# Performance work log

Hardware: AMD Instinct MI355X
Metric: run time of the kernel (lower is better)

The kernel has to match this reference:

```python
import jax, jax.numpy as jnp
import numpy as np

IN_SIZE = 1024
HIDDEN = 50
OUT_DIM = 8
BATCH = 16384
BN_EPS = 1e-5


def _gf(h, W1, b1, W2, b2):
    # graph_fusion: Linear -> LeakyReLU(0.2) -> Linear -> Tanh
    t = h @ W1 + b1
    t = jnp.where(t > 0, t, 0.2 * t)
    return jnp.tanh(t @ W2 + b2)


def _lrelu(z):
    return jnp.where(z > 0, z, 0.01 * z)  # F.leaky_relu default slope


def _dot(p, q):
    return jnp.sum(p * q, axis=-1)  # batched [B,1,D]@[B,D,1] -> [B]


def setup_inputs() -> dict:
    key = jax.random.key(0)
    ks = jax.random.split(key, 16)
    d, h, o = IN_SIZE, HIDDEN, OUT_DIM
    s = lambda n: 1.0 / np.sqrt(n)
    return {
        "x": jax.random.normal(ks[0], (BATCH, 3, d), jnp.float32),
        "att_W": jax.random.normal(ks[1], (d, 1), jnp.float32) * s(d),
        "att_b": jnp.zeros((1,), jnp.float32),
        "gf_W1": jax.random.normal(ks[2], (2 * d, 64), jnp.float32) * s(2 * d),
        "gf_b1": jnp.zeros((64,), jnp.float32),
        "gf_W2": jax.random.normal(ks[3], (64, d), jnp.float32) * s(64),
        "gf_b2": jnp.zeros((d,), jnp.float32),
        "bn_gamma": jnp.ones((3 * d,), jnp.float32),
        "bn_beta": jnp.zeros((3 * d,), jnp.float32),
        "l1_W": jax.random.normal(ks[4], (3 * d, h), jnp.float32) * s(3 * d),
        "l1_b": jnp.zeros((h,), jnp.float32),
        "l2_W": jax.random.normal(ks[5], (h, h), jnp.float32) * s(h),
        "l2_b": jnp.zeros((h,), jnp.float32),
        "l3_W": jax.random.normal(ks[6], (h, o), jnp.float32) * s(h),
        "l3_b": jnp.zeros((o,), jnp.float32),
    }


def _forward(x, att_W, att_b, gf_W1, gf_b1, gf_W2, gf_b2,
             bn_gamma, bn_beta, l1_W, l1_b, l2_W, l2_b, l3_W, l3_b):
    a1, v1, l1_ = x[:, 0, :], x[:, 1, :], x[:, 2, :]
    gf = lambda p, q: _gf(jnp.concatenate([p, q], axis=1), gf_W1, gf_b1, gf_W2, gf_b2)

    # unimodal attention weights, softmax over the 3 modalities
    att = jnp.tanh(x @ att_W + att_b)[..., 0]          # [B,3]
    w_uni = jax.nn.softmax(att, axis=1)                # [B,3]
    sa, sv, sl = w_uni[:, 0], w_uni[:, 1], w_uni[:, 2]
    unimodal = (sa[:, None] * a1 + sv[:, None] * v1 + sl[:, None] * l1_) / 3.0

    a = jax.nn.softmax(a1, axis=1)
    v = jax.nn.softmax(v1, axis=1)
    l = jax.nn.softmax(l1_, axis=1)
    sav = (sa + sv) / (_dot(a, v) + 0.5)
    sal = (sa + sl) / (_dot(a, l) + 0.5)
    svl = (sl + sv) / (_dot(v, l) + 0.5)
    w_bi = jax.nn.softmax(jnp.stack([sav, sal, svl], axis=1), axis=1)  # [B,3]

    a_v = _lrelu(w_bi[:, 0:1] * gf(a1, v1))
    a_l = _lrelu(w_bi[:, 1:2] * gf(a1, l1_))
    v_l = _lrelu(w_bi[:, 2:3] * gf(v1, l1_))
    bimodal = (a_v + a_l + v_l) / 3.0

    a_v2 = jax.nn.softmax(a_v, axis=1)
    a_l2 = jax.nn.softmax(a_l, axis=1)
    v_l2 = jax.nn.softmax(v_l, axis=1)
    savvl = (sav + svl) / (_dot(a_v2, v_l2) + 0.5)
    saavl = (sav + sal) / (_dot(a_v2, a_l2) + 0.5)
    savll = (sal + svl) / (_dot(a_l2, v_l2) + 0.5)
    savl = (sav + sl) / (_dot(a_v2, l) + 0.5)
    salv = (sal + sv) / (_dot(a_l2, v) + 0.5)
    svla = (sa + svl) / (_dot(v_l2, a) + 0.5)
    w_tri = jax.nn.softmax(
        jnp.stack([savvl, saavl, savll, savl, salv, svla], axis=1), axis=1)  # [B,6]

    avvl = _lrelu(w_tri[:, 0:1] * gf(a_v, v_l))
    aavl = _lrelu(w_tri[:, 1:2] * gf(a_v, a_l))
    avll = _lrelu(w_tri[:, 2:3] * gf(v_l, a_l))
    avl = _lrelu(w_tri[:, 3:4] * gf(a_v, l1_))
    alv = _lrelu(w_tri[:, 4:5] * gf(a_l, v1))
    vla = _lrelu(w_tri[:, 5:6] * gf(v_l, a1))
    trimodal = (avvl + aavl + avll + avl + alv + vla) / 6.0

    fusion = jnp.concatenate([unimodal, bimodal, trimodal], axis=1)  # [B,3*in]
    # BatchNorm1d in eval mode: running_mean=0, running_var=1
    fusion = fusion * (bn_gamma / jnp.sqrt(1.0 + BN_EPS)) + bn_beta
    y = jnp.tanh(fusion @ l1_W + l1_b)
    y = jnp.tanh(y @ l2_W + l2_b)
    y2 = jax.nn.softmax(y @ l3_W + l3_b, axis=1)
    total_weights = jnp.concatenate([w_uni, w_bi, w_tri], axis=1)  # [B,12]
    return y2, total_weights


def reference(x, att_W, att_b, gf_W1, gf_b1, gf_W2, gf_b2,
              bn_gamma, bn_beta, l1_W, l1_b, l2_W, l2_b, l3_W, l3_b):
    return _forward(x, att_W, att_b, gf_W1, gf_b1, gf_W2, gf_b2,
                    bn_gamma, bn_beta, l1_W, l1_b, l2_W, l2_b, l3_W, l3_b)
```

## Files before the change

kernel.cpp:

```cpp
#include <hip/hip_runtime.h>
#include <math.h>

#define NB 16384
#define DD 1024
#define KF 5120

typedef unsigned short u16;
typedef unsigned int u32;
typedef __attribute__((ext_vector_type(8))) short bf16x8;
typedef __attribute__((ext_vector_type(4))) float f32x4;

__device__ __forceinline__ float bf2f(u16 u){
  return __uint_as_float(((unsigned)u) << 16);
}
__device__ __forceinline__ u16 f2bf(float f){
  unsigned u = __float_as_uint(f);
  return (u16)((u + 0x7fffu + ((u >> 16) & 1u)) >> 16);
}
__device__ __forceinline__ u16 f2bf_tr(float f){
  return (u16)(__float_as_uint(f) >> 16);
}
__device__ __forceinline__ float fast_tanh(float x){
  float e = __expf(2.0f * x);
  return 1.0f - 2.0f * __builtin_amdgcn_rcpf(e + 1.0f);
}
__device__ __forceinline__ float wredsum(float x){
  #pragma unroll
  for(int o = 32; o >= 1; o >>= 1) x += __shfl_xor(x, o);
  return x;
}
__device__ __forceinline__ float wredmax(float x){
  #pragma unroll
  for(int o = 32; o >= 1; o >>= 1) x = fmaxf(x, __shfl_xor(x, o));
  return x;
}
__device__ __forceinline__ bf16x8 pack8f(float4 f0, float4 f1){
  bf16x8 r;
  r[0]=(short)f2bf(f0.x); r[1]=(short)f2bf(f0.y); r[2]=(short)f2bf(f0.z); r[3]=(short)f2bf(f0.w);
  r[4]=(short)f2bf(f1.x); r[5]=(short)f2bf(f1.y); r[6]=(short)f2bf(f1.z); r[7]=(short)f2bf(f1.w);
  return r;
}
__device__ __forceinline__ void gll16(const void* g, void* l){
  __builtin_amdgcn_global_load_lds(
      (const __attribute__((address_space(1))) u32*)g,
      (__attribute__((address_space(3))) u32*)l, 16, 0, 0);
}

__global__ __launch_bounds__(256) void k1_stats(
    const float* __restrict__ x, const float* __restrict__ attW,
    const float* __restrict__ attb, float* __restrict__ stats,
    u16* __restrict__ Fcat, float* __restrict__ tw)
{
  int wave = threadIdx.x >> 6, lane = threadIdx.x & 63;
  int r = blockIdx.x * 4 + wave;
  const float* xr = x + (size_t)r * 3 * DD;
  float a[16], v[16], l[16];
  float dA=0.f,dV=0.f,dL=0.f, mA=-1e30f,mV=-1e30f,mL=-1e30f;
  #pragma unroll
  for(int i = 0; i < 16; i++){
    int k = lane + i*64;
    a[i] = xr[k]; v[i] = xr[DD+k]; l[i] = xr[2*DD+k];
    float w = attW[k];
    dA = fmaf(a[i], w, dA); dV = fmaf(v[i], w, dV); dL = fmaf(l[i], w, dL);
    mA = fmaxf(mA, a[i]); mV = fmaxf(mV, v[i]); mL = fmaxf(mL, l[i]);
  }
  dA = wredsum(dA); dV = wredsum(dV); dL = wredsum(dL);
  mA = wredmax(mA); mV = wredmax(mV); mL = wredmax(mL);

  float Sa=0.f,Sv=0.f,Sl=0.f,Eav=0.f,Eal=0.f,Evl=0.f;
  #pragma unroll
  for(int i = 0; i < 16; i++){
    float ea = __expf(a[i]-mA), ev = __expf(v[i]-mV), el = __expf(l[i]-mL);
    Sa += ea; Sv += ev; Sl += el;
    Eav += ea*ev; Eal += ea*el; Evl += ev*el;
  }
  Sa = wredsum(Sa); Sv = wredsum(Sv); Sl = wredsum(Sl);
  Eav = wredsum(Eav); Eal = wredsum(Eal); Evl = wredsum(Evl);

  float ab = attb[0];
  float ta = fast_tanh(dA + ab), tv = fast_tanh(dV + ab), tl = fast_tanh(dL + ab);
  float mm = fmaxf(ta, fmaxf(tv, tl));
  float e0 = __expf(ta-mm), e1 = __expf(tv-mm), e2 = __expf(tl-mm);
  float ss = e0 + e1 + e2;
  float sa = e0/ss, sv = e1/ss, sl = e2/ss;
  float dav = Eav/(Sa*Sv), dal = Eal/(Sa*Sl), dvl = Evl/(Sv*Sl);
  float sav = (sa+sv)/(dav+0.5f);
  float sal = (sa+sl)/(dal+0.5f);
  float svl = (sv+sl)/(dvl+0.5f);
  float m2 = fmaxf(sav, fmaxf(sal, svl));
  float f0 = __expf(sav-m2), f1 = __expf(sal-m2), f2 = __expf(svl-m2);
  float s2 = f0 + f1 + f2;
  float wb0 = f0/s2, wb1 = f1/s2, wb2 = f2/s2;

  if(lane == 0){
    float* st = stats + (size_t)r*24;
    st[0]=sa; st[1]=sv; st[2]=sl;
    st[3]=wb0; st[4]=wb1; st[5]=wb2;
    st[6]=sav; st[7]=sal; st[8]=svl;
    st[9]=mA; st[10]=Sa; st[11]=mV; st[12]=Sv; st[13]=mL; st[14]=Sl;
    float* twr = tw + (size_t)r*12;
    twr[0]=sa; twr[1]=sv; twr[2]=sl; twr[3]=wb0; twr[4]=wb1; twr[5]=wb2;
  }
  #pragma unroll
  for(int i = 0; i < 16; i++){
    int k = lane + i*64;
    Fcat[(size_t)r*KF + k] = f2bf((sa*a[i] + sv*v[i] + sl*l[i]) * (1.0f/3.0f));
  }
}

__global__ __launch_bounds__(256) void kprew_b1(
    const float* __restrict__ W1, u16* __restrict__ Wb1)
{
  int idx = blockIdx.x * 256 + threadIdx.x;
  int n = idx >> 10, k = idx & 1023;
  float v = (n < 64) ? W1[(size_t)k*64 + n] : W1[(size_t)(1024+k)*64 + (n-64)];
  Wb1[idx] = f2bf(v);
}

__global__ __launch_bounds__(256) void kprew_w2t(
    const float* __restrict__ W2, u16* __restrict__ W2T)
{
  int idx = blockIdx.x * 256 + threadIdx.x;
  int c = idx >> 6, k = idx & 63;
  W2T[idx] = f2bf(W2[(size_t)k*DD + c]);
}

template<int FROM_X>
__global__ __launch_bounds__(256) void kg1v2(
    const float* __restrict__ xf, const u16* __restrict__ fc,
    const u16* __restrict__ Wb1, float* __restrict__ UV)
{
  __shared__ u16 Asm[2][64*64];
  int tid = threadIdx.x;
  int wv = tid >> 6, lane = tid & 63;
  int fr = lane & 15, kg = lane >> 4;
  int mb = blockIdx.x * 64;

  const u16* gsrc0 = nullptr; const u16* gsrc1 = nullptr;
  const float* xsrc0 = nullptr; const float* xsrc1 = nullptr;
  int rr_ = tid >> 3, pp_ = tid & 7;
  int sp_ = pp_ ^ (rr_ & 7);
  if(FROM_X){
    xsrc0 = xf + (size_t)(mb + rr_)*1024 + pp_*8;
    xsrc1 = xf + (size_t)(mb + rr_ + 32)*1024 + pp_*8;
  } else {
    int r8 = lane >> 3, p = lane & 7;
    int sp = p ^ (r8 & 7);
    int m0 = mb + (2*wv)*8 + r8;
    int m1 = mb + (2*wv+1)*8 + r8;
    int R0 = m0/3, R1 = m1/3;
    gsrc0 = fc + (size_t)R0*KF + (size_t)(1 + (m0 - 3*R0))*1024 + sp*8;
    gsrc1 = fc + (size_t)R1*KF + (size_t)(1 + (m1 - 3*R1))*1024 + sp*8;
  }

  f32x4 acc[4][2];
  #pragma unroll
  for(int rf = 0; rf < 4; rf++)
    #pragma unroll
    for(int nf = 0; nf < 2; nf++) acc[rf][nf] = (f32x4){0.f,0.f,0.f,0.f};

  if(FROM_X){
    float4 a0 = *(const float4*)xsrc0, a1 = *(const float4*)(xsrc0+4);
    float4 c0 = *(const float4*)xsrc1, c1 = *(const float4*)(xsrc1+4);
    *(bf16x8*)&Asm[0][rr_*64 + sp_*8]      = pack8f(a0,a1);
    *(bf16x8*)&Asm[0][(rr_+32)*64 + sp_*8] = pack8f(c0,c1);
  } else {
    gll16(gsrc0, &Asm[0][(2*wv)*512]);
    gll16(gsrc1, &Asm[0][(2*wv+1)*512]);
  }
  __syncthreads();

  int buf = 0;
  for(int ci = 0; ci < 16; ci++){
    int k0 = ci*64;
    float4 na0, na1, nc0, nc1;
    if(ci < 15){
      if(FROM_X){
        na0 = *(const float4*)(xsrc0 + k0 + 64); na1 = *(const float4*)(xsrc0 + k0 + 68);
        nc0 = *(const float4*)(xsrc1 + k0 + 64); nc1 = *(const float4*)(xsrc1 + k0 + 68);
      } else {
        gll16(gsrc0 + k0 + 64, &Asm[buf^1][(2*wv)*512]);
        gll16(gsrc1 + k0 + 64, &Asm[buf^1][(2*wv+1)*512]);
      }
    }
    #pragma unroll
    for(int ks = 0; ks < 2; ks++){
      bf16x8 a[4];
      #pragma unroll
      for(int rf = 0; rf < 4; rf++){
        int row = rf*16 + fr;
        int slot = (ks*4 + kg) ^ (fr & 7);
        a[rf] = *(const bf16x8*)&Asm[buf][row*64 + slot*8];
      }
      #pragma unroll
      for(int nf = 0; nf < 2; nf++){
        int col = wv*32 + nf*16 + fr;
        bf16x8 b = *(const bf16x8*)&Wb1[(size_t)col*1024 + k0 + ks*32 + kg*8];
        #pragma unroll
        for(int rf = 0; rf < 4; rf++)
          acc[rf][nf] = __builtin_amdgcn_mfma_f32_16x16x32_bf16(a[rf], b, acc[rf][nf], 0, 0, 0);
      }
    }
    if(FROM_X && ci < 15){
      *(bf16x8*)&Asm[buf^1][rr_*64 + sp_*8]      = pack8f(na0,na1);
      *(bf16x8*)&Asm[buf^1][(rr_+32)*64 + sp_*8] = pack8f(nc0,nc1);
    }
    __syncthreads();
    buf ^= 1;
  }

  #pragma unroll
  for(int rf = 0; rf < 4; rf++)
    #pragma unroll
    for(int nf = 0; nf < 2; nf++)
      #pragma unroll
      for(int q = 0; q < 4; q++)
        UV[(size_t)(mb + rf*16 + kg*4 + q)*128 + wv*32 + nf*16 + fr] = acc[rf][nf][q];
}

template<int P, int SUM>
__global__ __launch_bounds__(256) void kL2v2(
    const float* __restrict__ UVA, const float* __restrict__ UVB,
    const u16* __restrict__ W2T, const float* __restrict__ b1,
    const float* __restrict__ b2, const float* __restrict__ stats,
    u16* __restrict__ Fcat)
{
  __shared__ u16 Tsm[P][16][64];
  __shared__ float stw[16][8];
  int tid = threadIdx.x;
  int wv = tid >> 6, lane = tid & 63;
  int fr = lane & 15, kg = lane >> 4;
  int Rb = blockIdx.x * 16;
  int cb = blockIdx.y * 256 + wv * 64;

  const int NG = P*16*8;
  for(int i = tid; i < NG; i += 256){
    int g = i & 7, r = (i >> 3) & 15, p = i >> 7;
    int R = Rb + r;
    int up, vp; const float* VBb;
    if(P == 3){
      up = (p == 2) ? 1 : 0;
      vp = (p == 0) ? 1 : 2;
      VBb = UVA;
    } else {
      up = (0x210200 >> (p*4)) & 15;
      vp = (0x012112 >> (p*4)) & 15;
      VBb = (p < 3) ? UVA : UVB;
    }
    const float* Up = UVA + (size_t)(3*R + up)*128 + g*8;
    const float* Vp = VBb + (size_t)(3*R + vp)*128 + 64 + g*8;
    float4 u0 = *(const float4*)Up, u1 = *(const float4*)(Up+4);
    float4 v0 = *(const float4*)Vp, v1 = *(const float4*)(Vp+4);
    float4 bb0 = *(const float4*)(b1 + g*8), bb1 = *(const float4*)(b1 + g*8 + 4);
    float t[8] = {u0.x+v0.x+bb0.x, u0.y+v0.y+bb0.y, u0.z+v0.z+bb0.z, u0.w+v0.w+bb0.w,
                  u1.x+v1.x+bb1.x, u1.y+v1.y+bb1.y, u1.z+v1.z+bb1.z, u1.w+v1.w+bb1.w};
    bf16x8 o;
    #pragma unroll
    for(int j = 0; j < 8; j++){
      float tv = t[j] > 0.f ? t[j] : 0.2f*t[j];
      o[j] = (short)f2bf_tr(tv);
    }
    *(bf16x8*)&Tsm[p][r][(g ^ (r & 7))*8] = o;
  }
  if(tid < 16*P){
    int r = tid / P, p = tid - r*P;
    stw[r][p] = stats[(size_t)(Rb + r)*24 + (SUM ? 15 : 3) + p];
  }
  __syncthreads();

  f32x4 acc[P][4];
  #pragma unroll
  for(int p = 0; p < P; p++)
    #pragma unroll
    for(int cf = 0; cf < 4; cf++) acc[p][cf] = (f32x4){0.f,0.f,0.f,0.f};

  #pragma unroll
  for(int ks = 0; ks < 2; ks++){
    bf16x8 a[P];
    #pragma unroll
    for(int p = 0; p < P; p++)
      a[p] = *(const bf16x8*)&Tsm[p][fr][(((ks<<2)+kg) ^ (fr & 7))*8];
    #pragma unroll
    for(int cf = 0; cf < 4; cf++){
      bf16x8 b = *(const bf16x8*)&W2T[(size_t)(cb + cf*16 + fr)*64 + ks*32 + kg*8];
      #pragma unroll
      for(int p = 0; p < P; p++)
        acc[p][cf] = __builtin_amdgcn_mfma_f32_16x16x32_bf16(a[p], b, acc[p][cf], 0, 0, 0);
    }
  }

  #pragma unroll
  for(int q = 0; q < 4; q++){
    int Rq = Rb + kg*4 + q;
    #pragma unroll
    for(int cf = 0; cf < 4; cf++){
      int c = cb + cf*16 + fr;
      float b2c = b2[c];
      if(SUM){
        float s = 0.f;
        #pragma unroll
        for(int p = 0; p < P; p++){
          float g = stw[kg*4+q][p] * fast_tanh(acc[p][cf][q] + b2c);
          s += g > 0.f ? g : 0.01f*g;
        }
        Fcat[(size_t)Rq*KF + 4096 + c] = f2bf(s * (1.0f/6.0f));
      } else {
        #pragma unroll
        for(int p = 0; p < P; p++){
          float g = stw[kg*4+q][p] * fast_tanh(acc[p][cf][q] + b2c);
          float val = g > 0.f ? g : 0.01f*g;
          Fcat[(size_t)Rq*KF + (size_t)(1+p)*1024 + c] = f2bf(val);
        }
      }
    }
  }
}

__global__ __launch_bounds__(256) void k3s_stats2(
    const u16* __restrict__ Fcat, const float* __restrict__ x,
    float* __restrict__ stats, float* __restrict__ tw)
{
  int wave = threadIdx.x >> 6, lane = threadIdx.x & 63;
  int r = blockIdx.x * 4 + wave;
  const u16*   pv = Fcat + (size_t)r*KF + 1024;
  const float* xr = x    + (size_t)3*r*DD;
  float av[16], al[16], vl[16];
  float mav=-1e30f, mal=-1e30f, mvl=-1e30f;
  #pragma unroll
  for(int i = 0; i < 16; i++){
    int k = lane + i*64;
    av[i] = bf2f(pv[k]); al[i] = bf2f(pv[DD+k]); vl[i] = bf2f(pv[2*DD+k]);
    mav = fmaxf(mav, av[i]); mal = fmaxf(mal, al[i]); mvl = fmaxf(mvl, vl[i]);
  }
  mav = wredmax(mav); mal = wredmax(mal); mvl = wredmax(mvl);

  float* st = stats + (size_t)r*24;
  float sa=st[0], sv=st[1], sl=st[2];
  float sav=st[6], sal=st[7], svl=st[8];
  float mA=st[9], Sa=st[10], mV=st[11], Sv=st[12], mL=st[13], Sl=st[14];

  float Savv=0.f,Sall=0.f,Svll=0.f,E1=0.f,E2=0.f,E3=0.f,E4=0.f,E5=0.f,E6=0.f;
  #pragma unroll
  for(int i = 0; i < 16; i++){
    int k = lane + i*64;
    float a1 = xr[k], v1 = xr[DD+k], l1 = xr[2*DD+k];
    float eav = __expf(av[i]-mav), eal = __expf(al[i]-mal), evl = __expf(vl[i]-mvl);
    Savv += eav; Sall += eal; Svll += evl;
    float ea = __expf(a1-mA), ev = __expf(v1-mV), el = __expf(l1-mL);
    E1 += eav*evl; E2 += eav*eal; E3 += eal*evl;
    E4 += eav*el;  E5 += eal*ev;  E6 += evl*ea;
  }
  Savv = wredsum(Savv); Sall = wredsum(Sall); Svll = wredsum(Svll);
  E1 = wredsum(E1); E2 = wredsum(E2); E3 = wredsum(E3);
  E4 = wredsum(E4); E5 = wredsum(E5); E6 = wredsum(E6);

  float d1 = E1/(Savv*Svll), d2 = E2/(Savv*Sall), d3 = E3/(Sall*Svll);
  float d4 = E4/(Savv*Sl),   d5 = E5/(Sall*Sv),   d6 = E6/(Svll*Sa);
  float t0 = (sav+svl)/(d1+0.5f);
  float t1 = (sav+sal)/(d2+0.5f);
  float t2 = (sal+svl)/(d3+0.5f);
  float t3 = (sav+sl)/(d4+0.5f);
  float t4 = (sal+sv)/(d5+0.5f);
  float t5 = (sa+svl)/(d6+0.5f);
  float mx = fmaxf(fmaxf(fmaxf(t0,t1),fmaxf(t2,t3)),fmaxf(t4,t5));
  float g0=__expf(t0-mx),g1=__expf(t1-mx),g2=__expf(t2-mx);
  float g3=__expf(t3-mx),g4=__expf(t4-mx),g5=__expf(t5-mx);
  float gs = g0+g1+g2+g3+g4+g5;
  if(lane == 0){
    float wt[6] = {g0/gs,g1/gs,g2/gs,g3/gs,g4/gs,g5/gs};
    float* twr = tw + (size_t)r*12;
    #pragma unroll
    for(int p = 0; p < 6; p++){ st[15+p] = wt[p]; twr[6+p] = wt[p]; }
  }
}

__global__ __launch_bounds__(256) void k6_prew(
    const float* __restrict__ gamma, const float* __restrict__ l1W,
    u16* __restrict__ WpT)
{
  int kk = blockIdx.x * 256 + threadIdx.x;
  int j  = blockIdx.y;
  const float gsc = 1.0f / sqrtf(1.0f + 1e-5f);
  int korig; float sc;
  if(kk < 1024){ korig = kk; sc = 1.f; }
  else if(kk < 4096){ korig = 1024 + ((kk - 1024) & 1023); sc = 1.0f/3.0f; }
  else { korig = 2048 + (kk - 4096); sc = 1.f; }
  float v = (j < 50) ? l1W[(size_t)korig*50 + j] * gamma[korig] * gsc * sc : 0.f;
  WpT[(size_t)j*KF + kk] = f2bf(v);
}

__global__ __launch_bounds__(256) void k6_preb(
    const float* __restrict__ beta, const float* __restrict__ l1W,
    const float* __restrict__ l1b, float* __restrict__ bp)
{
  __shared__ float red[4][64];
  int j = threadIdx.x & 63, seg = threadIdx.x >> 6;
  float s = 0.f;
  if(j < 50){
    for(int k = seg*768; k < seg*768 + 768; k++)
      s = fmaf(beta[k], l1W[(size_t)k*50 + j], s);
  }
  red[seg][j] = s;
  __syncthreads();
  if(seg == 0){
    float t = red[0][j] + red[1][j] + red[2][j] + red[3][j];
    bp[j] = (j < 50) ? (l1b[j] + t) : 0.f;
  }
}

__global__ __launch_bounds__(256) void k6v3(
    const u16* __restrict__ Fcat, const u16* __restrict__ WpT,
    const float* __restrict__ bp,
    const float* __restrict__ l2W, const float* __restrict__ l2b,
    const float* __restrict__ l3W, const float* __restrict__ l3b,
    float* __restrict__ y2out)
{
  __shared__ __align__(16) char smem[29760];
  u16*  Asm = (u16*)smem;
  float* W2s = (float*)(smem + 8192);
  float* W3s = (float*)(smem + 8192 + 12800);
  float* Ys  = (float*)smem;
  float* Ys2 = (float*)(smem + 8192 + 12800 + 1600);

  int tid = threadIdx.x;
  int wv = tid >> 6, lane = tid & 63;
  int fr = lane & 15, kg = lane >> 4;
  int rb = blockIdx.x * 32;

  for(int t = tid; t < 3200; t += 256){
    int c = t & 63;
    W2s[t] = (c < 50) ? l2W[(t >> 6)*50 + c] : 0.f;
  }
  for(int t = tid; t < 400; t += 256) W3s[t] = l3W[t];

  int r8 = lane >> 3, pp = lane & 7;
  int sp = pp ^ r8;
  const u16* gsrc = Fcat + (size_t)(rb + wv*8 + r8)*KF + sp*8;
  const u16* bptr = WpT  + (size_t)(fr)*KF + (size_t)wv*16*KF + kg*8;

  f32x4 acc[2];
  acc[0] = (f32x4){0.f,0.f,0.f,0.f};
  acc[1] = (f32x4){0.f,0.f,0.f,0.f};

  gll16(gsrc, &Asm[wv*512]);
  __syncthreads();

  int buf = 0;
  for(int ci = 0; ci < 80; ci++){
    int k0 = ci*64;
    if(ci < 79)
      gll16(gsrc + k0 + 64, &Asm[(buf^1)*2048 + wv*512]);
    #pragma unroll
    for(int ks = 0; ks < 2; ks++){
      bf16x8 b = *(const bf16x8*)(bptr + k0 + ks*32);
      #pragma unroll
      for(int rf = 0; rf < 2; rf++){
        int row = rf*16 + fr;
        int slot = (ks*4 + kg) ^ (fr & 7);
        bf16x8 a = *(const bf16x8*)&Asm[buf*2048 + row*64 + slot*8];
        acc[rf] = __builtin_amdgcn_mfma_f32_16x16x32_bf16(a, b, acc[rf], 0, 0, 0);
      }
    }
    __syncthreads();
    buf ^= 1;
  }

  {
    int col = wv*16 + fr;
    float bpc = bp[col];
    #pragma unroll
    for(int rf = 0; rf < 2; rf++)
      #pragma unroll
      for(int q = 0; q < 4; q++){
        int row = rf*16 + kg*4 + q;
        if(col < 50) Ys[row*56 + col] = fast_tanh(acc[rf][q] + bpc);
      }
  }
  __syncthreads();

  {
    int r = tid >> 3, cg = (tid & 7) * 7;
    float a2[7] = {0,0,0,0,0,0,0};
    for(int k = 0; k < 50; k++){
      float yv = Ys[r*56 + k];
      #pragma unroll
      for(int c = 0; c < 7; c++) a2[c] = fmaf(yv, W2s[k*64 + cg + c], a2[c]);
    }
    #pragma unroll
    for(int c = 0; c < 7; c++){
      int cc = cg + c;
      if(cc < 50) Ys2[r*56 + cc] = fast_tanh(a2[c] + l2b[cc]);
    }
  }
  __syncthreads();

  {
    int r = tid >> 3, c = tid & 7;
    float z = l3b[c];
    for(int k = 0; k < 50; k++) z = fmaf(Ys2[r*56 + k], W3s[k*8 + c], z);
    float m = z;
    m = fmaxf(m, __shfl_xor(m, 1));
    m = fmaxf(m, __shfl_xor(m, 2));
    m = fmaxf(m, __shfl_xor(m, 4));
    float e = __expf(z - m);
    float s = e;
    s += __shfl_xor(s, 1); s += __shfl_xor(s, 2); s += __shfl_xor(s, 4);
    y2out[(size_t)(rb + r)*8 + c] = e / s;
  }
}

extern "C" void kernel_launch(void* const* d_in, const int* in_sizes, int n_in,
                              void* d_out, int out_size, void* d_ws, size_t ws_size,
                              hipStream_t stream)
{
  (void)in_sizes; (void)n_in; (void)out_size; (void)ws_size;
  const float* x    = (const float*)d_in[0];
  const float* attW = (const float*)d_in[1];
  const float* attb = (const float*)d_in[2];
  const float* gfW1 = (const float*)d_in[3];
  const float* gfb1 = (const float*)d_in[4];
  const float* gfW2 = (const float*)d_in[5];
  const float* gfb2 = (const float*)d_in[6];
  const float* bng  = (const float*)d_in[7];
  const float* bnb  = (const float*)d_in[8];
  const float* l1W  = (const float*)d_in[9];
  const float* l1b  = (const float*)d_in[10];
  const float* l2W  = (const float*)d_in[11];
  const float* l2b  = (const float*)d_in[12];
  const float* l3W  = (const float*)d_in[13];
  const float* l3b  = (const float*)d_in[14];

  float* out = (float*)d_out;
  float* tw  = out + (size_t)NB*8;

  float* ws    = (float*)d_ws;
  float* stats = ws;
  float* UV1   = stats + (size_t)NB*24;
  float* UV2   = UV1 + (size_t)3*NB*128;
  float* bp    = UV2 + (size_t)3*NB*128;
  u16* WpT     = (u16*)(bp + 64);
  u16* Wb1     = WpT + (size_t)64*KF;
  u16* W2T     = Wb1 + (size_t)128*1024;
  u16* Fcat    = W2T + (size_t)1024*64;

  k1_stats<<<dim3(NB/4), dim3(256), 0, stream>>>(x, attW, attb, stats, Fcat, tw);
  kprew_b1<<<dim3(512), dim3(256), 0, stream>>>(gfW1, Wb1);
  kprew_w2t<<<dim3(256), dim3(256), 0, stream>>>(gfW2, W2T);
  k6_prew<<<dim3(20, 64), dim3(256), 0, stream>>>(bng, l1W, WpT);
  k6_preb<<<dim3(1), dim3(256), 0, stream>>>(bnb, l1W, l1b, bp);

  kg1v2<1><<<dim3(3*NB/64), dim3(256), 0, stream>>>(x, (const u16*)nullptr, Wb1, UV1);
  kL2v2<3,0><<<dim3(NB/16, 4), dim3(256), 0, stream>>>(UV1, UV1, W2T, gfb1, gfb2, stats, Fcat);
  k3s_stats2<<<dim3(NB/4), dim3(256), 0, stream>>>(Fcat, x, stats, tw);
  kg1v2<0><<<dim3(3*NB/64), dim3(256), 0, stream>>>((const float*)nullptr, Fcat, Wb1, UV2);
  kL2v2<6,1><<<dim3(NB/16, 4), dim3(256), 0, stream>>>(UV2, UV1, W2T, gfb1, gfb2, stats, Fcat);
  k6v3<<<dim3(NB/32), dim3(256), 0, stream>>>(Fcat, WpT, bp, l2W, l2b, l3W, l3b, out);
}
```

Before: 424.5 us.

## Stage gf outputs through LDS for coalesced stores and vectorize stats loads

kL2v2 is replaced by kL2v3. Each block now covers all 1024 columns for its 16 rows by looping over four column groups, so the T-tile gather and A-fragment loads happen once per block instead of once per column quarter. Results are staged in a padded LDS buffer and written to Fcat as 16-byte vectors, replacing scattered 2-byte stores. The stats kernels k1_stats and k3s_stats2 switch to float2 and packed-bf16 loads and stores to halve the number of memory instructions. The cost is a quarter as many blocks for the kL2 launches, extra barriers, and more LDS per block, which may lower occupancy.

```diff
diff --git a/kernel.cpp b/kernel.cpp
--- a/kernel.cpp
+++ b/kernel.cpp
@@ -19,6 +19,9 @@
 }
 __device__ __forceinline__ u16 f2bf_tr(float f){
   return (u16)(__float_as_uint(f) >> 16);
+}
+__device__ __forceinline__ u32 pack2bf(float a, float b){
+  return (u32)f2bf(a) | ((u32)f2bf(b) << 16);
 }
 __device__ __forceinline__ float fast_tanh(float x){
   float e = __expf(2.0f * x);
@@ -53,26 +56,33 @@
 {
   int wave = threadIdx.x >> 6, lane = threadIdx.x & 63;
   int r = blockIdx.x * 4 + wave;
-  const float* xr = x + (size_t)r * 3 * DD;
-  float a[16], v[16], l[16];
+  const float2* xr  = (const float2*)(x + (size_t)r * 3 * DD);
+  const float2* aw2 = (const float2*)attW;
+  float2 a[8], v[8], l[8];
   float dA=0.f,dV=0.f,dL=0.f, mA=-1e30f,mV=-1e30f,mL=-1e30f;
   #pragma unroll
-  for(int i = 0; i < 16; i++){
-    int k = lane + i*64;
-    a[i] = xr[k]; v[i] = xr[DD+k]; l[i] = xr[2*DD+k];
-    float w = attW[k];
-    dA = fmaf(a[i], w, dA); dV = fmaf(v[i], w, dV); dL = fmaf(l[i], w, dL);
-    mA = fmaxf(mA, a[i]); mV = fmaxf(mV, v[i]); mL = fmaxf(mL, l[i]);
+  for(int i = 0; i < 8; i++){
+    int k2 = lane + i*64;
+    a[i] = xr[k2]; v[i] = xr[512+k2]; l[i] = xr[1024+k2];
+    float2 w = aw2[k2];
+    dA = fmaf(a[i].x, w.x, fmaf(a[i].y, w.y, dA));
+    dV = fmaf(v[i].x, w.x, fmaf(v[i].y, w.y, dV));
+    dL = fmaf(l[i].x, w.x, fmaf(l[i].y, w.y, dL));
+    mA = fmaxf(mA, fmaxf(a[i].x, a[i].y));
+    mV = fmaxf(mV, fmaxf(v[i].x, v[i].y));
+    mL = fmaxf(mL, fmaxf(l[i].x, l[i].y));
   }
   dA = wredsum(dA); dV = wredsum(dV); dL = wredsum(dL);
   mA = wredmax(mA); mV = wredmax(mV); mL = wredmax(mL);
 
   float Sa=0.f,Sv=0.f,Sl=0.f,Eav=0.f,Eal=0.f,Evl=0.f;
   #pragma unroll
-  for(int i = 0; i < 16; i++){
-    float ea = __expf(a[i]-mA), ev = __expf(v[i]-mV), el = __expf(l[i]-mL);
-    Sa += ea; Sv += ev; Sl += el;
-    Eav += ea*ev; Eal += ea*el; Evl += ev*el;
+  for(int i = 0; i < 8; i++){
+    float eax = __expf(a[i].x-mA), eay = __expf(a[i].y-mA);
+    float evx = __expf(v[i].x-mV), evy = __expf(v[i].y-mV);
+    float elx = __expf(l[i].x-mL), ely = __expf(l[i].y-mL);
+    Sa += eax+eay; Sv += evx+evy; Sl += elx+ely;
+    Eav += eax*evx + eay*evy; Eal += eax*elx + eay*ely; Evl += evx*elx + evy*ely;
   }
   Sa = wredsum(Sa); Sv = wredsum(Sv); Sl = wredsum(Sl);
   Eav = wredsum(Eav); Eal = wredsum(Eal); Evl = wredsum(Evl);
@@ -101,10 +111,13 @@
     float* twr = tw + (size_t)r*12;
     twr[0]=sa; twr[1]=sv; twr[2]=sl; twr[3]=wb0; twr[4]=wb1; twr[5]=wb2;
   }
-  #pragma unroll
-  for(int i = 0; i < 16; i++){
-    int k = lane + i*64;
-    Fcat[(size_t)r*KF + k] = f2bf((sa*a[i] + sv*v[i] + sl*l[i]) * (1.0f/3.0f));
+  u32* uniw = (u32*)(Fcat + (size_t)r*KF);
+  #pragma unroll
+  for(int i = 0; i < 8; i++){
+    int k2 = lane + i*64;
+    float ux = (sa*a[i].x + sv*v[i].x + sl*l[i].x) * (1.0f/3.0f);
+    float uy = (sa*a[i].y + sv*v[i].y + sl*l[i].y) * (1.0f/3.0f);
+    uniw[k2] = pack2bf(ux, uy);
   }
 }
 
@@ -219,19 +232,20 @@
 }
 
 template<int P, int SUM>
-__global__ __launch_bounds__(256) void kL2v2(
+__global__ __launch_bounds__(256) void kL2v3(
     const float* __restrict__ UVA, const float* __restrict__ UVB,
     const u16* __restrict__ W2T, const float* __restrict__ b1,
     const float* __restrict__ b2, const float* __restrict__ stats,
     u16* __restrict__ Fcat)
 {
+  const int NP = SUM ? 1 : P;
   __shared__ u16 Tsm[P][16][64];
+  __shared__ u16 Osm[SUM?1:P][16][264];
   __shared__ float stw[16][8];
   int tid = threadIdx.x;
   int wv = tid >> 6, lane = tid & 63;
   int fr = lane & 15, kg = lane >> 4;
   int Rb = blockIdx.x * 16;
-  int cb = blockIdx.y * 256 + wv * 64;
 
   const int NG = P*16*8;
   for(int i = tid; i < NG; i += 256){
@@ -268,50 +282,67 @@
   }
   __syncthreads();
 
-  f32x4 acc[P][4];
-  #pragma unroll
-  for(int p = 0; p < P; p++)
-    #pragma unroll
-    for(int cf = 0; cf < 4; cf++) acc[p][cf] = (f32x4){0.f,0.f,0.f,0.f};
-
-  #pragma unroll
-  for(int ks = 0; ks < 2; ks++){
-    bf16x8 a[P];
+  bf16x8 afr[2][P];
+  #pragma unroll
+  for(int ks = 0; ks < 2; ks++)
     #pragma unroll
     for(int p = 0; p < P; p++)
-      a[p] = *(const bf16x8*)&Tsm[p][fr][(((ks<<2)+kg) ^ (fr & 7))*8];
-    #pragma unroll
-    for(int cf = 0; cf < 4; cf++){
-      bf16x8 b = *(const bf16x8*)&W2T[(size_t)(cb + cf*16 + fr)*64 + ks*32 + kg*8];
-      #pragma unroll
-      for(int p = 0; p < P; p++)
-        acc[p][cf] = __builtin_amdgcn_mfma_f32_16x16x32_bf16(a[p], b, acc[p][cf], 0, 0, 0);
-    }
-  }
-
-  #pragma unroll
-  for(int q = 0; q < 4; q++){
-    int Rq = Rb + kg*4 + q;
-    #pragma unroll
-    for(int cf = 0; cf < 4; cf++){
-      int c = cb + cf*16 + fr;
-      float b2c = b2[c];
-      if(SUM){
-        float s = 0.f;
+      afr[ks][p] = *(const bf16x8*)&Tsm[p][fr][(((ks<<2)+kg) ^ (fr & 7))*8];
+
+  int orow = tid >> 4, oc16 = (tid & 15) * 16;
+
+  for(int cg = 0; cg < 4; cg++){
+    int cb = cg*256 + wv*64;
+    f32x4 acc[P][4];
+    #pragma unroll
+    for(int p = 0; p < P; p++)
+      #pragma unroll
+      for(int cf = 0; cf < 4; cf++) acc[p][cf] = (f32x4){0.f,0.f,0.f,0.f};
+
+    #pragma unroll
+    for(int ks = 0; ks < 2; ks++)
+      #pragma unroll
+      for(int cf = 0; cf < 4; cf++){
+        bf16x8 b = *(const bf16x8*)&W2T[(size_t)(cb + cf*16 + fr)*64 + ks*32 + kg*8];
         #pragma unroll
-        for(int p = 0; p < P; p++){
-          float g = stw[kg*4+q][p] * fast_tanh(acc[p][cf][q] + b2c);
-          s += g > 0.f ? g : 0.01f*g;
+        for(int p = 0; p < P; p++)
+          acc[p][cf] = __builtin_amdgcn_mfma_f32_16x16x32_bf16(afr[ks][p], b, acc[p][cf], 0, 0, 0);
+      }
+
+    if(cg > 0) __syncthreads();
+    #pragma unroll
+    for(int q = 0; q < 4; q++){
+      int row = kg*4 + q;
+      #pragma unroll
+      for(int cf = 0; cf < 4; cf++){
+        int cloc = wv*64 + cf*16 + fr;
+        float b2c = b2[cg*256 + cloc];
+        if(SUM){
+          float s = 0.f;
+          #pragma unroll
+          for(int p = 0; p < P; p++){
+            float g = stw[row][p] * fast_tanh(acc[p][cf][q] + b2c);
+            s += g > 0.f ? g : 0.01f*g;
+          }
+          Osm[0][row][cloc] = f2bf(s * (1.0f/6.0f));
+        } else {
+          #pragma unroll
+          for(int p = 0; p < P; p++){
+            float g = stw[row][p] * fast_tanh(acc[p][cf][q] + b2c);
+            float val = g > 0.f ? g : 0.01f*g;
+            Osm[p][row][cloc] = f2bf(val);
+          }
         }
-        Fcat[(size_t)Rq*KF + 4096 + c] = f2bf(s * (1.0f/6.0f));
-      } else {
-        #pragma unroll
-        for(int p = 0; p < P; p++){
-          float g = stw[kg*4+q][p] * fast_tanh(acc[p][cf][q] + b2c);
-          float val = g > 0.f ? g : 0.01f*g;
-          Fcat[(size_t)Rq*KF + (size_t)(1+p)*1024 + c] = f2bf(val);
-        }
-      }
+      }
+    }
+    __syncthreads();
+    #pragma unroll
+    for(int p = 0; p < NP; p++){
+      bf16x8 o0 = *(const bf16x8*)&Osm[p][orow][oc16];
+      bf16x8 o1 = *(const bf16x8*)&Osm[p][orow][oc16 + 8];
+      size_t off = (size_t)(Rb + orow)*KF + (SUM ? 4096 : (size_t)(1+p)*1024) + cg*256 + oc16;
+      *(bf16x8*)&Fcat[off]     = o0;
+      *(bf16x8*)&Fcat[off + 8] = o1;
     }
   }
 }
@@ -322,15 +353,20 @@
 {
   int wave = threadIdx.x >> 6, lane = threadIdx.x & 63;
   int r = blockIdx.x * 4 + wave;
-  const u16*   pv = Fcat + (size_t)r*KF + 1024;
-  const float* xr = x    + (size_t)3*r*DD;
-  float av[16], al[16], vl[16];
+  const u32* pv = (const u32*)(Fcat + (size_t)r*KF + 1024);
+  const float2* xr = (const float2*)(x + (size_t)3*r*DD);
+  float2 av[8], al[8], vl[8];
   float mav=-1e30f, mal=-1e30f, mvl=-1e30f;
   #pragma unroll
-  for(int i = 0; i < 16; i++){
-    int k = lane + i*64;
-    av[i] = bf2f(pv[k]); al[i] = bf2f(pv[DD+k]); vl[i] = bf2f(pv[2*DD+k]);
-    mav = fmaxf(mav, av[i]); mal = fmaxf(mal, al[i]); mvl = fmaxf(mvl, vl[i]);
+  for(int i = 0; i < 8; i++){
+    int k2 = lane + i*64;
+    u32 wa = pv[k2], wb = pv[512+k2], wc = pv[1024+k2];
+    av[i] = make_float2(bf2f((u16)wa), bf2f((u16)(wa>>16)));
+    al[i] = make_float2(bf2f((u16)wb), bf2f((u16)(wb>>16)));
+    vl[i] = make_float2(bf2f((u16)wc), bf2f((u16)(wc>>16)));
+    mav = fmaxf(mav, fmaxf(av[i].x, av[i].y));
+    mal = fmaxf(mal, fmaxf(al[i].x, al[i].y));
+    mvl = fmaxf(mvl, fmaxf(vl[i].x, vl[i].y));
   }
   mav = wredmax(mav); mal = wredmax(mal); mvl = wredmax(mvl);
 
@@ -341,14 +377,18 @@
 
   float Savv=0.f,Sall=0.f,Svll=0.f,E1=0.f,E2=0.f,E3=0.f,E4=0.f,E5=0.f,E6=0.f;
   #pragma unroll
-  for(int i = 0; i < 16; i++){
-    int k = lane + i*64;
-    float a1 = xr[k], v1 = xr[DD+k], l1 = xr[2*DD+k];
-    float eav = __expf(av[i]-mav), eal = __expf(al[i]-mal), evl = __expf(vl[i]-mvl);
-    Savv += eav; Sall += eal; Svll += evl;
-    float ea = __expf(a1-mA), ev = __expf(v1-mV), el = __expf(l1-mL);
-    E1 += eav*evl; E2 += eav*eal; E3 += eal*evl;
-    E4 += eav*el;  E5 += eal*ev;  E6 += evl*ea;
+  for(int i = 0; i < 8; i++){
+    int k2 = lane + i*64;
+    float2 a1 = xr[k2], v1 = xr[512+k2], l1 = xr[1024+k2];
+    float eavx = __expf(av[i].x-mav), eavy = __expf(av[i].y-mav);
+    float ealx = __expf(al[i].x-mal), ealy = __expf(al[i].y-mal);
+    float evlx = __expf(vl[i].x-mvl), evly = __expf(vl[i].y-mvl);
+    Savv += eavx+eavy; Sall += ealx+ealy; Svll += evlx+evly;
+    float eax = __expf(a1.x-mA), eay = __expf(a1.y-mA);
+    float evx = __expf(v1.x-mV), evy = __expf(v1.y-mV);
+    float elx = __expf(l1.x-mL), ely = __expf(l1.y-mL);
+    E1 += eavx*evlx + eavy*evly; E2 += eavx*ealx + eavy*ealy; E3 += ealx*evlx + ealy*evly;
+    E4 += eavx*elx + eavy*ely;   E5 += ealx*evx + ealy*evy;   E6 += evlx*eax + evly*eay;
   }
   Savv = wredsum(Savv); Sall = wredsum(Sall); Svll = wredsum(Svll);
   E1 = wredsum(E1); E2 = wredsum(E2); E3 = wredsum(E3);
@@ -550,9 +590,9 @@
   k6_preb<<<dim3(1), dim3(256), 0, stream>>>(bnb, l1W, l1b, bp);
 
   kg1v2<1><<<dim3(3*NB/64), dim3(256), 0, stream>>>(x, (const u16*)nullptr, Wb1, UV1);
-  kL2v2<3,0><<<dim3(NB/16, 4), dim3(256), 0, stream>>>(UV1, UV1, W2T, gfb1, gfb2, stats, Fcat);
+  kL2v3<3,0><<<dim3(NB/16), dim3(256), 0, stream>>>(UV1, UV1, W2T, gfb1, gfb2, stats, Fcat);
   k3s_stats2<<<dim3(NB/4), dim3(256), 0, stream>>>(Fcat, x, stats, tw);
   kg1v2<0><<<dim3(3*NB/64), dim3(256), 0, stream>>>((const float*)nullptr, Fcat, Wb1, UV2);
-  kL2v2<6,1><<<dim3(NB/16, 4), dim3(256), 0, stream>>>(UV2, UV1, W2T, gfb1, gfb2, stats, Fcat);
+  kL2v3<6,1><<<dim3(NB/16), dim3(256), 0, stream>>>(UV2, UV1, W2T, gfb1, gfb2, stats, Fcat);
   k6v3<<<dim3(NB/32), dim3(256), 0, stream>>>(Fcat, WpT, bp, l2W, l2b, l3W, l3b, out);
 }
```

Result: slower. 450.0 us (+6.0%).
